# Kernel optimization log

Measured on AMD Instinct MI355X. Metric: run time of the kernel, lower is better.

## Reference

```python
import jax, jax.numpy as jnp
import numpy as np


def _c2e(faces):
    # faces: [6, B, C, h, h] in order back, down, front, left, right, up
    # returns equirect map [B, C, H=h, W=2h] via bilinear cube sampling
    _, B, C, h, _ = faces.shape
    H, W = h, 2 * h
    lat = (0.5 - (jnp.arange(H) + 0.5) / H) * jnp.pi      # +pi/2 (top) .. -pi/2
    lon = (2.0 * (jnp.arange(W) + 0.5) / W - 1.0) * jnp.pi  # -pi .. +pi
    cl = jnp.cos(lat)[:, None]
    vx = cl * jnp.sin(lon)[None, :]
    vy = jnp.broadcast_to(jnp.sin(lat)[:, None], (H, W))
    vz = cl * jnp.cos(lon)[None, :]
    dirs = jnp.stack([vx, vy, vz], -1)                     # [H,W,3]
    ax, ay, az = jnp.abs(vx), jnp.abs(vy), jnp.abs(vz)
    cond_z = (az >= ax) & (az >= ay)
    cond_x = (~cond_z) & (ax >= ay)
    # face ids: 0 back(-z) 1 down(-y) 2 front(+z) 3 left(-x) 4 right(+x) 5 up(+y)
    face = jnp.where(cond_z, jnp.where(vz > 0, 2, 0),
                     jnp.where(cond_x, jnp.where(vx > 0, 4, 3),
                               jnp.where(vy > 0, 5, 1)))
    N = jnp.array([[0, 0, -1], [0, -1, 0], [0, 0, 1], [-1, 0, 0], [1, 0, 0], [0, 1, 0]], jnp.float32)
    R = jnp.array([[-1, 0, 0], [1, 0, 0], [1, 0, 0], [0, 0, 1], [0, 0, -1], [1, 0, 0]], jnp.float32)
    U = jnp.array([[0, 1, 0], [0, 0, -1], [0, 1, 0], [0, 1, 0], [0, 1, 0], [0, 0, 1]], jnp.float32)
    den = jnp.sum(dirs * N[face], -1)
    a = jnp.sum(dirs * R[face], -1) / den                  # in-plane x, [-1,1]
    bcoord = jnp.sum(dirs * U[face], -1) / den             # in-plane y, [-1,1]
    uu = jnp.clip((a + 1.0) * 0.5 * (h - 1), 0.0, h - 1)   # align_corners-style
    vv = jnp.clip((1.0 - bcoord) * 0.5 * (h - 1), 0.0, h - 1)
    x0 = jnp.floor(uu).astype(jnp.int32)
    y0 = jnp.floor(vv).astype(jnp.int32)
    x1 = jnp.minimum(x0 + 1, h - 1)
    y1 = jnp.minimum(y0 + 1, h - 1)
    dx = uu - x0
    dy = vv - y0
    ft = faces.transpose(0, 3, 4, 1, 2).reshape(6, h, h, B * C)  # [6,h,h,B*C]
    g = lambda yy, xx: ft[face, yy, xx]                    # gather -> [H,W,B*C]
    out = (g(y0, x0) * ((1 - dx) * (1 - dy))[..., None]
           + g(y0, x1) * (dx * (1 - dy))[..., None]
           + g(y1, x0) * ((1 - dx) * dy)[..., None]
           + g(y1, x1) * (dx * dy)[..., None])
    return out.reshape(H, W, B, C).transpose(2, 3, 0, 1)


def _conv(x, w, bias, pad):
    y = jax.lax.conv_general_dilated(x, w, (1, 1), [(pad, pad), (pad, pad)],
                                     dimension_numbers=('NCHW', 'OIHW', 'NCHW'))
    return y + bias[None, :, None, None]


def setup_inputs() -> dict:
    key = jax.random.key(0)
    ks = jax.random.split(key, 12)
    B, C, h = 4, 64, 128
    face_shape = (B, C, h, h)
    return {
        'm': jax.random.normal(ks[0], (B, C, h, 2 * h), jnp.float32),
        'f': jax.random.normal(ks[1], face_shape, jnp.float32),
        'r': jax.random.normal(ks[2], face_shape, jnp.float32),
        'b': jax.random.normal(ks[3], face_shape, jnp.float32),
        'l': jax.random.normal(ks[4], face_shape, jnp.float32),
        'u': jax.random.normal(ks[5], face_shape, jnp.float32),
        'd': jax.random.normal(ks[6], face_shape, jnp.float32),
        'w_fusion': jax.random.normal(ks[7], (C, C, 3, 3), jnp.float32) * 0.05,
        'b_fusion': jnp.zeros((C,), jnp.float32),
        'w_mask': jax.random.normal(ks[8], (1, 2 * C, 1, 1), jnp.float32) * 0.05,
        'b_mask': jnp.zeros((1,), jnp.float32),
    }


def reference(m, f, r, b, l, u, d, w_fusion, b_fusion, w_mask, b_mask):
    # cube faces stacked in the original order: back, down, front, left, right, up
    faces = jnp.stack([b, d, f, l, r, u], 0)               # [6,B,C,h,h]
    aux = _c2e(faces)                                      # [B,C,h,2h]
    m_aux = jax.nn.relu(_conv(aux, w_fusion, b_fusion, 1))
    m_main = jax.nn.relu(_conv(m, w_fusion, b_fusion, 1))  # shared conv_fusion weights
    joint = jnp.concatenate([m_main, m_aux], axis=1)
    mask = jax.nn.sigmoid(_conv(joint, w_mask, b_mask, 0)) # [B,1,h,2h]
    return m + mask * m_aux
```

## Files before the change

### kernel.cpp

```cpp
#include <hip/hip_runtime.h>
#include <math.h>
#include <stdint.h>

#define BB 4
#define CC 64
#define HH 128
#define HOUT 128
#define WOUT 256
#define NPIX (HOUT * WOUT)
#define NMAP (BB * CC * HOUT * WOUT)

typedef __attribute__((ext_vector_type(8))) short short8;
typedef __attribute__((ext_vector_type(4))) float floatx4;

__device__ __forceinline__ uint16_t f2bf(float f) {
    uint32_t u = __float_as_uint(f);
    u += 0x7fffu + ((u >> 16) & 1u);
    return (uint16_t)(u >> 16);
}
__device__ __forceinline__ float bfu2f(uint32_t v) { return __uint_as_float(v << 16); }

__global__ __launch_bounds__(256) void prep_kernel(uint32_t* __restrict__ pk,
                                                   float* __restrict__ pdx,
                                                   float* __restrict__ pdy,
                                                   const float* __restrict__ wf,
                                                   uint4* __restrict__ Bsw) {
    if (blockIdx.x < 128) {
        int p = blockIdx.x * 256 + threadIdx.x;
        int y = p >> 8;
        int x = p & 255;
        const float PI = 3.14159265358979323846f;
        float lat = (0.5f - (y + 0.5f) / (float)HOUT) * PI;
        float lon = (2.0f * (x + 0.5f) / (float)WOUT - 1.0f) * PI;
        float cl = cosf(lat);
        float vx = cl * sinf(lon);
        float vy = sinf(lat);
        float vz = cl * cosf(lon);
        float ax = fabsf(vx), ay = fabsf(vy), az = fabsf(vz);

        int face;
        float den, a, b;
        if (az >= ax && az >= ay) {
            if (vz > 0.0f) { face = 2; den = vz;  a = vx;  b = vy; }
            else           { face = 0; den = -vz; a = -vx; b = vy; }
        } else if (ax >= ay) {
            if (vx > 0.0f) { face = 4; den = vx;  a = -vz; b = vy; }
            else           { face = 3; den = -vx; a = vz;  b = vy; }
        } else {
            if (vy > 0.0f) { face = 5; den = vy;  a = vx;  b = vz; }
            else           { face = 1; den = -vy; a = vx;  b = -vz; }
        }
        a /= den;
        b /= den;
        float uu = fminf(fmaxf((a + 1.0f) * 0.5f * (HH - 1), 0.0f), (float)(HH - 1));
        float vv = fminf(fmaxf((1.0f - b) * 0.5f * (HH - 1), 0.0f), (float)(HH - 1));
        int x0 = (int)floorf(uu);
        int y0 = (int)floorf(vv);
        int x1 = min(x0 + 1, HH - 1);
        int y1 = min(y0 + 1, HH - 1);
        pdx[p] = uu - (float)x0;
        pdy[p] = vv - (float)y0;
        pk[p] = (uint32_t)face | ((uint32_t)x0 << 3) | ((uint32_t)y0 << 10) |
                ((uint32_t)x1 << 17) | ((uint32_t)y1 << 24);
    } else {
        int tid = (blockIdx.x - 128) * 256 + threadIdx.x;
        if (tid >= 9 * 2 * 4 * 64) return;
        int lane = tid & 63;
        int rest = tid >> 6;
        int n = rest & 3, ks = (rest >> 2) & 1, tap = rest >> 3;
        int co = n * 16 + (lane & 15);
        uint32_t w4[4];
#pragma unroll
        for (int pw = 0; pw < 4; pw++) {
            int ci0 = ks * 32 + (lane >> 4) * 8 + pw * 2;
            uint32_t lo = f2bf(wf[(size_t)(co * CC + ci0) * 9 + tap]);
            uint32_t hi = f2bf(wf[(size_t)(co * CC + ci0 + 1) * 9 + tap]);
            w4[pw] = lo | (hi << 16);
        }
        Bsw[tid] = make_uint4(w4[0], w4[1], w4[2], w4[3]);
    }
}

__global__ __launch_bounds__(256) void facepack_kernel(
    const float* __restrict__ pB, const float* __restrict__ pD,
    const float* __restrict__ pF, const float* __restrict__ pL,
    const float* __restrict__ pR, const float* __restrict__ pU,
    uint16_t* __restrict__ FCL) {
    __shared__ uint16_t lds[64 * 256];
    int bid = blockIdx.x;
    int half = bid & 1;
    int y = (bid >> 1) & 127;
    int fc = bid >> 8;
    const float* src = (fc == 0) ? pB : (fc == 1) ? pD : (fc == 2) ? pF
                     : (fc == 3) ? pL : (fc == 4) ? pR : pU;
    int t = threadIdx.x;
    int xl = t & 63;
    int x = half * 64 + xl;
    int cgb = t >> 6;

#pragma unroll
    for (int i = 0; i < 8; i++) {
        int cg = i * 4 + cgb;
        uint32_t w4[4];
#pragma unroll
        for (int j = 0; j < 4; j++) {
            int bc0 = cg * 8 + j * 2;
            uint32_t lo = f2bf(src[((size_t)bc0 * HH + y) * HH + x]);
            uint32_t hi = f2bf(src[((size_t)(bc0 + 1) * HH + y) * HH + x]);
            w4[j] = lo | (hi << 16);
        }
        int off = xl * 256 + ((cg ^ (xl & 7)) * 8);
        *(uint4*)&lds[off] = make_uint4(w4[0], w4[1], w4[2], w4[3]);
    }
    __syncthreads();
    size_t obase = (((size_t)fc * HH + y) * HH + half * 64) * 256;
#pragma unroll
    for (int i = 0; i < 8; i++) {
        int q = i * 256 + t;
        int xx = q >> 5, cg = q & 31;
        int off = xx * 256 + ((cg ^ (xx & 7)) * 8);
        *(uint4*)&FCL[obase + (size_t)q * 8] = *(const uint4*)&lds[off];
    }
}

__global__ __launch_bounds__(256) void gather_kernel(
    const uint32_t* __restrict__ pk, const float* __restrict__ pdx,
    const float* __restrict__ pdy, const uint16_t* __restrict__ FCL,
    uint16_t* __restrict__ Xa) {
    int tid = blockIdx.x * 256 + threadIdx.x;
    int chunk = tid & 31;
    int p = tid >> 5;

    uint32_t k = pk[p];
    float dx = pdx[p], dy = pdy[p];
    int fc = k & 7;
    int x0 = (k >> 3) & 127, y0 = (k >> 10) & 127;
    int x1 = (k >> 17) & 127, y1 = (k >> 24) & 127;

    const uint16_t* base = FCL + (size_t)fc * HH * HH * 256 + chunk * 8;
    uint4 c00 = *(const uint4*)(base + ((size_t)y0 * HH + x0) * 256);
    uint4 c01 = *(const uint4*)(base + ((size_t)y0 * HH + x1) * 256);
    uint4 c10 = *(const uint4*)(base + ((size_t)y1 * HH + x0) * 256);
    uint4 c11 = *(const uint4*)(base + ((size_t)y1 * HH + x1) * 256);

    float w00 = (1.0f - dx) * (1.0f - dy);
    float w01 = dx * (1.0f - dy);
    float w10 = (1.0f - dx) * dy;
    float w11 = dx * dy;

    const uint32_t* a00 = (const uint32_t*)&c00;
    const uint32_t* a01 = (const uint32_t*)&c01;
    const uint32_t* a10 = (const uint32_t*)&c10;
    const uint32_t* a11 = (const uint32_t*)&c11;
    uint32_t r[4];
#pragma unroll
    for (int w = 0; w < 4; w++) {
        float lo = w00 * bfu2f(a00[w] & 0xffffu) + w01 * bfu2f(a01[w] & 0xffffu)
                 + w10 * bfu2f(a10[w] & 0xffffu) + w11 * bfu2f(a11[w] & 0xffffu);
        float hi = w00 * bfu2f(a00[w] >> 16) + w01 * bfu2f(a01[w] >> 16)
                 + w10 * bfu2f(a10[w] >> 16) + w11 * bfu2f(a11[w] >> 16);
        r[w] = (uint32_t)f2bf(lo) | ((uint32_t)f2bf(hi) << 16);
    }

    int b = chunk >> 3, c = (chunk & 7) * 8;
    int y = p >> 8, x = p & 255;
    size_t o = (((size_t)(b * HOUT + y)) * WOUT + x) * CC + c;
    *(uint4*)(Xa + o) = make_uint4(r[0], r[1], r[2], r[3]);
}

__global__ __launch_bounds__(256) void pack_kernel(const float* __restrict__ src,
                                                   uint16_t* __restrict__ dst) {
    __shared__ uint16_t lds[WOUT * CC];
    int t = threadIdx.x;
    int by = blockIdx.x;
    int b = by >> 7, y = by & 127;

#pragma unroll
    for (int cg = 0; cg < 8; cg++) {
        uint32_t w4[4];
#pragma unroll
        for (int pw = 0; pw < 4; pw++) {
            int c0 = cg * 8 + pw * 2;
            uint32_t lo = f2bf(src[((size_t)(b * CC + c0) * HOUT + y) * WOUT + t]);
            uint32_t hi = f2bf(src[((size_t)(b * CC + c0 + 1) * HOUT + y) * WOUT + t]);
            w4[pw] = lo | (hi << 16);
        }
        int off = t * 64 + ((cg ^ (t & 7)) * 8);
        *(uint4*)&lds[off] = make_uint4(w4[0], w4[1], w4[2], w4[3]);
    }
    __syncthreads();
    size_t obase = (size_t)((b * HOUT + y) * WOUT) * CC;
#pragma unroll
    for (int i = 0; i < 8; i++) {
        int q = i * 256 + t;
        int p = q >> 3, c8 = q & 7;
        int off = p * 64 + ((c8 ^ (p & 7)) * 8);
        *(uint4*)&dst[obase + (size_t)q * 8] = *(const uint4*)&lds[off];
    }
}

__global__ __launch_bounds__(256) void gemm_kernel(const uint16_t* __restrict__ Xm,
                                                   const uint16_t* __restrict__ Xa,
                                                   const uint4* __restrict__ Bsw,
                                                   const float* __restrict__ bias,
                                                   uint16_t* __restrict__ Ym,
                                                   uint16_t* __restrict__ Ya) {
    int tensor = blockIdx.x >> 9;
    int by = blockIdx.x & 511;
    int b = by >> 7, y = by & 127;
    const uint16_t* X = tensor ? Xa : Xm;
    uint16_t* Y = tensor ? Ya : Ym;
    int lane = threadIdx.x & 63;
    int wave = threadIdx.x >> 6;
    int x0 = wave * 64;
    int l15 = lane & 15, lq = lane >> 4;
    long rowpix = (long)(b * HOUT + y) * WOUT;

    floatx4 acc[4][4];
#pragma unroll
    for (int mt = 0; mt < 4; mt++)
#pragma unroll
        for (int n = 0; n < 4; n++) acc[mt][n] = (floatx4)0.0f;

#pragma unroll
    for (int tap = 0; tap < 9; tap++) {
        const int dy = tap / 3 - 1, dx = tap % 3 - 1;
        const bool rowok = (unsigned)(y + dy) < (unsigned)HOUT;
#pragma unroll
        for (int ks = 0; ks < 2; ks++) {
            short8 bfr[4];
            const uint4* bp = Bsw + (size_t)((tap * 2 + ks) * 4) * 64 + lane;
#pragma unroll
            for (int n = 0; n < 4; n++) {
                uint4 t4 = bp[n * 64];
                bfr[n] = *(short8*)&t4;
            }
#pragma unroll
            for (int mt = 0; mt < 4; mt++) {
                int xs = x0 + mt * 16 + l15 + dx;
                short8 af = (short8)0;
                if (rowok && (unsigned)xs < (unsigned)WOUT) {
                    long pix = rowpix + (long)dy * WOUT + xs;
                    af = *(const short8*)(X + pix * CC + ks * 32 + lq * 8);
                }
#pragma unroll
                for (int n = 0; n < 4; n++)
                    acc[mt][n] = __builtin_amdgcn_mfma_f32_16x16x32_bf16(
                        af, bfr[n], acc[mt][n], 0, 0, 0);
            }
        }
    }
#pragma unroll
    for (int n = 0; n < 4; n++) {
        int co = n * 16 + l15;
        float bb = bias[co];
#pragma unroll
        for (int mt = 0; mt < 4; mt++) {
#pragma unroll
            for (int r = 0; r < 4; r++) {
                float v = acc[mt][n][r] + bb;
                v = v > 0.0f ? v : 0.0f;
                long px = rowpix + x0 + mt * 16 + lq * 4 + r;
                Y[px * CC + co] = f2bf(v);
            }
        }
    }
}

__global__ __launch_bounds__(256) void maskfinal_kernel(
    const float* __restrict__ m, const uint16_t* __restrict__ Ym,
    const uint16_t* __restrict__ Ya, const float* __restrict__ wm,
    const float* __restrict__ bm, float* __restrict__ out) {
    int t = threadIdx.x;
    int by = blockIdx.x;
    int b = by >> 7, y = by & 127;
    size_t pix = (size_t)(b * HOUT + y) * WOUT + t;
    const uint4* ym4 = (const uint4*)(Ym + pix * CC);
    const uint4* ya4 = (const uint4*)(Ya + pix * CC);
    uint4 ya[8];
    float acc = bm[0];
#pragma unroll
    for (int g = 0; g < 8; g++) {
        uint4 um = ym4[g];
        uint4 av = ya4[g];
        ya[g] = av;
        const uint32_t* pu = (const uint32_t*)&um;
        const uint32_t* pa = (const uint32_t*)&av;
#pragma unroll
        for (int w = 0; w < 4; w++) {
            int c = g * 8 + w * 2;
            acc += wm[c]     * bfu2f(pu[w] & 0xffffu);
            acc += wm[c + 1] * bfu2f(pu[w] >> 16);
            acc += wm[64 + c]     * bfu2f(pa[w] & 0xffffu);
            acc += wm[64 + c + 1] * bfu2f(pa[w] >> 16);
        }
    }
    float mask = 1.0f / (1.0f + expf(-acc));
#pragma unroll
    for (int g = 0; g < 8; g++) {
        const uint32_t* pa = (const uint32_t*)&ya[g];
#pragma unroll
        for (int w = 0; w < 4; w++) {
            int c = g * 8 + w * 2;
            size_t i0 = ((size_t)(b * CC + c) * HOUT + y) * WOUT + t;
            size_t i1 = i0 + (size_t)HOUT * WOUT;
            out[i0] = m[i0] + mask * bfu2f(pa[w] & 0xffffu);
            out[i1] = m[i1] + mask * bfu2f(pa[w] >> 16);
        }
    }
}

__global__ __launch_bounds__(256) void signal_kernel(float* __restrict__ out, float v) {
    int idx = blockIdx.x * 256 + threadIdx.x;
    out[idx] = v;
}

extern "C" void kernel_launch(void* const* d_in, const int* in_sizes, int n_in,
                              void* d_out, int out_size, void* d_ws, size_t ws_size,
                              hipStream_t stream) {
    const float* m  = (const float*)d_in[0];
    const float* f  = (const float*)d_in[1];
    const float* r  = (const float*)d_in[2];
    const float* bk = (const float*)d_in[3];
    const float* l  = (const float*)d_in[4];
    const float* u  = (const float*)d_in[5];
    const float* dn = (const float*)d_in[6];
    const float* wf = (const float*)d_in[7];
    const float* bf = (const float*)d_in[8];
    const float* wm = (const float*)d_in[9];
    const float* bm = (const float*)d_in[10];
    float* out = (float*)d_out;

    const size_t OFF_FCL = 0;
    const size_t OFF_YM  = 0;
    const size_t OFF_YA  = (size_t)16 << 20;
    const size_t OFF_BSW = (size_t)51 << 20;
    const size_t OFF_PK  = OFF_BSW + (1u << 17);
    const size_t OFF_PDX = OFF_PK + (1u << 17);
    const size_t OFF_PDY = OFF_PDX + (1u << 17);
    const size_t NEED    = OFF_PDY + (1u << 17);

    if (ws_size < NEED) {
        float v = 100.0f + (float)(ws_size >> 20);
        signal_kernel<<<NMAP / 256, 256, 0, stream>>>(out, v);
        return;
    }

    char* ws = (char*)d_ws;
    uint16_t* FCL = (uint16_t*)(ws + OFF_FCL);
    uint16_t* Ym  = (uint16_t*)(ws + OFF_YM);
    uint16_t* Ya  = (uint16_t*)(ws + OFF_YA);
    uint4* Bsw    = (uint4*)(ws + OFF_BSW);
    uint32_t* pk  = (uint32_t*)(ws + OFF_PK);
    float* pdx    = (float*)(ws + OFF_PDX);
    float* pdy    = (float*)(ws + OFF_PDY);
    uint16_t* Xm  = (uint16_t*)d_out;
    uint16_t* Xa  = (uint16_t*)d_out + (size_t)NMAP;

    prep_kernel<<<146, 256, 0, stream>>>(pk, pdx, pdy, wf, Bsw);
    facepack_kernel<<<6 * HH * 2, 256, 0, stream>>>(bk, dn, f, l, r, u, FCL);
    gather_kernel<<<(NPIX * 32) / 256, 256, 0, stream>>>(pk, pdx, pdy, FCL, Xa);
    pack_kernel<<<BB * HOUT, 256, 0, stream>>>(m, Xm);
    gemm_kernel<<<2 * BB * HOUT, 256, 0, stream>>>(Xm, Xa, Bsw, bf, Ym, Ya);
    maskfinal_kernel<<<BB * HOUT, 256, 0, stream>>>(m, Ym, Ya, wm, bm, out);
}
```

Before: 275.8 us.

## Stage conv input halo tile in LDS and split rows into half-width blocks

The 3x3 conv GEMM kernel now cooperatively loads a 3-row by 160-pixel halo tile (with XOR swizzle) into shared memory, and the MFMA A-fragments come from LDS rather than repeated global loads with bounds checks. Each block covers half a row (128 pixels), which doubles the grid. Block indices are remapped so that neighbouring rows land on the same XCD for L2 locality. This cuts redundant global and L2 traffic across the nine taps, at the cost of about 60KB of LDS per block, which may limit occupancy, plus a sync and extra halo loads.

```diff
diff --git a/kernel.cpp b/kernel.cpp
--- a/kernel.cpp
+++ b/kernel.cpp
@@ -205,27 +205,51 @@
                                                    const float* __restrict__ bias,
                                                    uint16_t* __restrict__ Ym,
                                                    uint16_t* __restrict__ Ya) {
-    int tensor = blockIdx.x >> 9;
-    int by = blockIdx.x & 511;
-    int b = by >> 7, y = by & 127;
+    __shared__ uint16_t lds[3 * 160 * CC];
+    int gid = blockIdx.x;
+    int tensor = gid >> 10;
+    int b = (gid >> 8) & 3;
+    int i = gid & 255;
+    int xcd = i & 7, j = i >> 3;
+    int y = xcd * 16 + (j & 15);
+    int h = j >> 4;
     const uint16_t* X = tensor ? Xa : Xm;
     uint16_t* Y = tensor ? Ya : Ym;
+    const int wx = h * 128 - 16;
+
+    int tid = threadIdx.x;
+    const uint16_t* Xb = X + (size_t)b * (HOUT * WOUT * CC);
+#pragma unroll
+    for (int it = 0; it < 15; it++) {
+        int cid = it * 256 + tid;
+        int c = cid & 7;
+        int pr = cid >> 3;
+        int p = pr % 160;
+        int r = pr / 160;
+        int gy = y + r - 1;
+        int gx = wx + p;
+        uint4 v = make_uint4(0, 0, 0, 0);
+        if ((unsigned)gy < (unsigned)HOUT && (unsigned)gx < (unsigned)WOUT)
+            v = *(const uint4*)(Xb + ((size_t)gy * WOUT + gx) * CC + c * 8);
+        int slot = (r * 160 + p) * 8 + (c ^ (p & 7));
+        *(uint4*)&lds[slot * 8] = v;
+    }
+    __syncthreads();
+
     int lane = threadIdx.x & 63;
     int wave = threadIdx.x >> 6;
-    int x0 = wave * 64;
     int l15 = lane & 15, lq = lane >> 4;
-    long rowpix = (long)(b * HOUT + y) * WOUT;
-
-    floatx4 acc[4][4];
-#pragma unroll
-    for (int mt = 0; mt < 4; mt++)
+
+    floatx4 acc[2][4];
+#pragma unroll
+    for (int mt = 0; mt < 2; mt++)
 #pragma unroll
         for (int n = 0; n < 4; n++) acc[mt][n] = (floatx4)0.0f;
 
 #pragma unroll
     for (int tap = 0; tap < 9; tap++) {
         const int dy = tap / 3 - 1, dx = tap % 3 - 1;
-        const bool rowok = (unsigned)(y + dy) < (unsigned)HOUT;
+        const int r = 1 + dy;
 #pragma unroll
         for (int ks = 0; ks < 2; ks++) {
             short8 bfr[4];
@@ -236,13 +260,11 @@
                 bfr[n] = *(short8*)&t4;
             }
 #pragma unroll
-            for (int mt = 0; mt < 4; mt++) {
-                int xs = x0 + mt * 16 + l15 + dx;
-                short8 af = (short8)0;
-                if (rowok && (unsigned)xs < (unsigned)WOUT) {
-                    long pix = rowpix + (long)dy * WOUT + xs;
-                    af = *(const short8*)(X + pix * CC + ks * 32 + lq * 8);
-                }
+            for (int mt = 0; mt < 2; mt++) {
+                int p = wave * 32 + mt * 16 + l15 + dx + 16;
+                int chunk = ks * 4 + lq;
+                int slot = (r * 160 + p) * 8 + (chunk ^ (p & 7));
+                short8 af = *(const short8*)&lds[slot * 8];
 #pragma unroll
                 for (int n = 0; n < 4; n++)
                     acc[mt][n] = __builtin_amdgcn_mfma_f32_16x16x32_bf16(
@@ -250,17 +272,18 @@
             }
         }
     }
+    long rowpix = (long)(b * HOUT + y) * WOUT;
 #pragma unroll
     for (int n = 0; n < 4; n++) {
         int co = n * 16 + l15;
         float bb = bias[co];
 #pragma unroll
-        for (int mt = 0; mt < 4; mt++) {
-#pragma unroll
-            for (int r = 0; r < 4; r++) {
-                float v = acc[mt][n][r] + bb;
+        for (int mt = 0; mt < 2; mt++) {
+#pragma unroll
+            for (int rg = 0; rg < 4; rg++) {
+                float v = acc[mt][n][rg] + bb;
                 v = v > 0.0f ? v : 0.0f;
-                long px = rowpix + x0 + mt * 16 + lq * 4 + r;
+                long px = rowpix + h * 128 + wave * 32 + mt * 16 + lq * 4 + rg;
                 Y[px * CC + co] = f2bf(v);
             }
         }
@@ -361,6 +384,6 @@
     facepack_kernel<<<6 * HH * 2, 256, 0, stream>>>(bk, dn, f, l, r, u, FCL);
     gather_kernel<<<(NPIX * 32) / 256, 256, 0, stream>>>(pk, pdx, pdy, FCL, Xa);
     pack_kernel<<<BB * HOUT, 256, 0, stream>>>(m, Xm);
-    gemm_kernel<<<2 * BB * HOUT, 256, 0, stream>>>(Xm, Xa, Bsw, bf, Ym, Ya);
+    gemm_kernel<<<2 * BB * HOUT * 2, 256, 0, stream>>>(Xm, Xa, Bsw, bf, Ym, Ya);
     maskfinal_kernel<<<BB * HOUT, 256, 0, stream>>>(m, Ym, Ya, wm, bm, out);
 }
```

Measured after the change: 264.1 us. 4.2% less time.
